# Optimization experiments

Measured on AMD Instinct MI355X. Metric: run time of the kernel, lower is better.

## Reference

```python
import jax, jax.numpy as jnp
import numpy as np

N, D, H1, H2 = 8192, 768, 512, 256


def _nig_head(x, W1, b1, W2, b2, Wh, bh):
    # Linear -> GELU -> (dropout=id) -> Linear -> GELU -> Linear head, then softplus transforms
    h = jax.nn.gelu(x @ W1 + b1, approximate=False)
    h = jax.nn.gelu(h @ W2 + b2, approximate=False)
    r = h @ Wh + bh  # [N, 4]
    mu = r[:, 0]
    v = jax.nn.softplus(r[:, 1]) + 1e-6
    a = jax.nn.softplus(r[:, 2]) + 1.0 + 1e-6
    b = jax.nn.softplus(r[:, 3]) + 1e-6
    return mu, v, a, b


def setup_inputs() -> dict:
    key = jax.random.key(0)
    ks = jax.random.split(key, 16)
    f32 = jnp.float32
    sd = 1.0 / np.sqrt(D)

    def lin(k, din, dout):
        kw, kb = jax.random.split(k)
        W = jax.random.normal(kw, (din, dout), f32) * (1.0 / np.sqrt(din))
        b = jax.random.normal(kb, (dout,), f32) * 0.01
        return W, b

    X = jax.random.normal(ks[0], (N, D), f32)
    Wq = jax.random.normal(ks[1], (D, D), f32) * sd
    Wk = jax.random.normal(ks[2], (D, D), f32) * sd
    Wg, bg = lin(ks[3], D, D)
    gam = jnp.array(1.0, f32)
    ih_W1, ih_b1 = lin(ks[4], D, H1)
    ih_W2, ih_b2 = lin(ks[5], H1, H2)
    ih_Wh, ih_bh = lin(ks[6], H2, 4)
    fh_W1, fh_b1 = lin(ks[7], D, H1)
    fh_W2, fh_b2 = lin(ks[8], H1, H2)
    fh_Wh, fh_bh = lin(ks[9], H2, 4)
    return {
        "X": X, "Wq": Wq, "Wk": Wk, "Wg": Wg, "bg": bg, "gam": gam,
        "ih_W1": ih_W1, "ih_b1": ih_b1, "ih_W2": ih_W2, "ih_b2": ih_b2,
        "ih_Wh": ih_Wh, "ih_bh": ih_bh,
        "fh_W1": fh_W1, "fh_b1": fh_b1, "fh_W2": fh_W2, "fh_b2": fh_b2,
        "fh_Wh": fh_Wh, "fh_bh": fh_bh,
    }


def reference(X, Wq, Wk, Wg, bg, gam,
              ih_W1, ih_b1, ih_W2, ih_b2, ih_Wh, ih_bh,
              fh_W1, fh_b1, fh_W2, fh_b2, fh_Wh, fh_bh):
    # initial NIG head -> epistemic uncertainty -> gate
    m0, v0, a0, b0 = _nig_head(X, ih_W1, ih_b1, ih_W2, ih_b2, ih_Wh, ih_bh)
    u0 = b0 / jnp.maximum(a0 - 1.0, 1e-8)
    G = 1.0 - gam * jax.nn.sigmoid(u0)  # [N]

    # dense attention adjacency
    scale = jnp.sqrt(jnp.asarray(D, X.dtype))
    Q = X @ Wq
    K = X @ Wk
    A = jax.nn.softmax(Q @ K.T / scale, axis=-1)  # [N, N]

    # uncertainty outer-product gate + row renormalization
    A_gated = A * G[None, :] * G[:, None]
    Dinv = 1.0 / jnp.maximum(A_gated.sum(-1, keepdims=True), 1e-8)

    # degree-normalized GCN aggregation + linear + GELU
    M = jax.nn.gelu((A_gated * Dinv) @ X @ Wg + bg, approximate=False)

    # final NIG head on residual
    mu, v, al, be = _nig_head(X + M, fh_W1, fh_b1, fh_W2, fh_b2, fh_Wh, fh_bh)
    return (m0, v0, a0, b0, mu, v, al, be)
```

## Files before the change

### kernel.cpp

```cpp
#include <hip/hip_runtime.h>
#include <hip/hip_bf16.h>
#include <hip/hip_fp8.h>
#include <math.h>
#include <stdint.h>
#include <stddef.h>


#define NT    8192
#define DD    768
#define DH1   512
#define DH2   256
#define PANEL 4096
#define NPAN  (NT / PANEL)

typedef __attribute__((ext_vector_type(8))) short  short8;
typedef __attribute__((ext_vector_type(4))) float  f32x4;
typedef __attribute__((ext_vector_type(2))) long   longx2;

#define MFMA16(a, b, c) __builtin_amdgcn_mfma_f32_16x16x32_bf16((a), (b), (c), 0, 0, 0)
#define MFMAF8(a, b, c) __builtin_amdgcn_mfma_f32_16x16x32_fp8_fp8((a), (b), (c), 0, 0, 0)

__device__ __forceinline__ float bf2f(__hip_bfloat16 x) { return __bfloat162float(x); }
__device__ __forceinline__ __hip_bfloat16 f2bf(float x) { return __float2bfloat16(x); }
__device__ __forceinline__ uint8_t f2fp8(float x) { return __hip_fp8_e4m3(x).__x; }

__device__ __forceinline__ float gelu_f(float x) {
    return 0.5f * x * (1.0f + erff(x * 0.7071067811865476f));
}
__device__ __forceinline__ float softplus_f(float x) {
    return (x > 20.0f) ? x : log1pf(expf(x));
}

__device__ __forceinline__ void gload16(const void* g, void* l) {
    __builtin_amdgcn_global_load_lds(
        (const __attribute__((address_space(1))) void*)g,
        (__attribute__((address_space(3))) void*)l, 16, 0, 0);
}

template <int N>
__device__ __forceinline__ void wait_barrier() {
    asm volatile("s_waitcnt vmcnt(%0)\n\ts_barrier" :: "i"(N) : "memory");
}
__device__ __forceinline__ void plain_barrier() {
    asm volatile("s_barrier" ::: "memory");
}

__device__ __forceinline__ void xcd_remap(int& bx, int& by) {
    const int nbx = gridDim.x, nby = gridDim.y;
    if ((nby & 7) == 0) {
        const int lin = by * nbx + bx;
        const int x   = lin & 7;
        const int s   = lin >> 3;
        bx = s % nbx;
        by = x + 8 * (s / nbx);
    }
}

template <int EPI, bool SPLIT, int TM, int TN>
__global__ __launch_bounds__(256)
void gemm_bt(const __hip_bfloat16* __restrict__ Ahi, const __hip_bfloat16* __restrict__ Alo, int lda,
             const __hip_bfloat16* __restrict__ Bhi, const __hip_bfloat16* __restrict__ Blo, int ldb,
             __hip_bfloat16* __restrict__ obf_hi, __hip_bfloat16* __restrict__ obf_lo,
             uint8_t* __restrict__ of8, int ldc,
             const float* __restrict__ bias, int K)
{
    constexpr int NB  = SPLIT ? 2 : 1;
    constexpr int WRM = (TM == 128 && TN == 128) ? 2 : (TM == 128 ? 4 : 2);
    constexpr int WCN = 4 / WRM;
    constexpr int WTM = TM / WRM;
    constexpr int WTN = TN / WCN;
    constexpr int MI  = WTM / 16;
    constexpr int NI  = WTN / 16;
    constexpr int PA  = TM / 64;
    constexpr int PB  = TN / 64;
    constexpr int LPI = (PA + PB) * NB;

    __shared__ __align__(16) __hip_bfloat16 As[NB][3][TM * 32];
    __shared__ __align__(16) __hip_bfloat16 Bs[NB][3][TN * 32];

    const int tid  = threadIdx.x;
    const int wave = tid >> 6;
    const int lane = tid & 63;
    int bx = blockIdx.x, by = blockIdx.y;
    xcd_remap(bx, by);
    const int tm = by * TM;
    const int tn = bx * TN;

    const int srow  = tid >> 2;
    const int sgcol = ((tid & 3) ^ ((srow >> 1) & 3)) * 8;
    const int lofs  = srow * 32 + (tid & 3) * 8;

    size_t aoffs[PA], boffs[PB];
#pragma unroll
    for (int p = 0; p < PA; ++p) aoffs[p] = (size_t)(tm + p * 64 + srow) * lda + sgcol;
#pragma unroll
    for (int p = 0; p < PB; ++p) boffs[p] = (size_t)(tn + p * 64 + srow) * ldb + sgcol;

    auto stage = [&](int k0, int buf) {
#pragma unroll
        for (int p = 0; p < PA; ++p)
            gload16(Ahi + aoffs[p] + k0, &As[0][buf][p * 2048 + lofs]);
#pragma unroll
        for (int p = 0; p < PB; ++p)
            gload16(Bhi + boffs[p] + k0, &Bs[0][buf][p * 2048 + lofs]);
        if constexpr (SPLIT) {
#pragma unroll
            for (int p = 0; p < PA; ++p)
                gload16(Alo + aoffs[p] + k0, &As[1][buf][p * 2048 + lofs]);
#pragma unroll
            for (int p = 0; p < PB; ++p)
                gload16(Blo + boffs[p] + k0, &Bs[1][buf][p * 2048 + lofs]);
        }
    };

    f32x4 acc[MI][NI];
#pragma unroll
    for (int i = 0; i < MI; ++i)
#pragma unroll
        for (int j = 0; j < NI; ++j) {
            f32x4 z = {0.0f, 0.0f, 0.0f, 0.0f};
            acc[i][j] = z;
        }

    const int wm   = (wave / WCN) * WTM;
    const int wn   = (wave % WCN) * WTN;
    const int l16  = lane & 15;
    const int quad = lane >> 4;
    const int rchunk = (quad ^ ((l16 >> 1) & 3)) * 8;
    const int arow0  = (wm + l16) * 32 + rchunk;
    const int brow0  = (wn + l16) * 32 + rchunk;

    const int nIter = K >> 5;
    stage(0, 0);
    if (nIter > 1) stage(32, 1);
    for (int k = 0; k < nIter; ++k) {
        const int cb = k % 3;
        if (k + 2 < nIter) {
            stage((k + 2) << 5, (k + 2) % 3);
            wait_barrier<2 * LPI>();
        } else if (k + 1 < nIter) {
            wait_barrier<LPI>();
        } else {
            wait_barrier<0>();
        }

        short8 ah[MI], bh[NI];
#pragma unroll
        for (int i = 0; i < MI; ++i) ah[i] = *(const short8*)&As[0][cb][arow0 + i * 512];
#pragma unroll
        for (int j = 0; j < NI; ++j) bh[j] = *(const short8*)&Bs[0][cb][brow0 + j * 512];
        if constexpr (SPLIT) {
            short8 al[MI], bl[NI];
#pragma unroll
            for (int i = 0; i < MI; ++i) al[i] = *(const short8*)&As[1][cb][arow0 + i * 512];
#pragma unroll
            for (int j = 0; j < NI; ++j) bl[j] = *(const short8*)&Bs[1][cb][brow0 + j * 512];
#pragma unroll
            for (int mi = 0; mi < MI; ++mi)
#pragma unroll
                for (int ni = 0; ni < NI; ++ni) {
                    acc[mi][ni] = MFMA16(ah[mi], bh[ni], acc[mi][ni]);
                    acc[mi][ni] = MFMA16(ah[mi], bl[ni], acc[mi][ni]);
                    acc[mi][ni] = MFMA16(al[mi], bh[ni], acc[mi][ni]);
                }
        } else {
#pragma unroll
            for (int mi = 0; mi < MI; ++mi)
#pragma unroll
                for (int ni = 0; ni < NI; ++ni)
                    acc[mi][ni] = MFMA16(ah[mi], bh[ni], acc[mi][ni]);
        }
        plain_barrier();
    }

    const int rbase = tm + wm + quad * 4;
    const int cbase = tn + wn + l16;

    if constexpr (EPI == 0) {
#pragma unroll
        for (int mi = 0; mi < MI; ++mi)
#pragma unroll
            for (int ni = 0; ni < NI; ++ni) {
                f32x4 v = acc[mi][ni];
                const int col = cbase + ni * 16;
#pragma unroll
                for (int r = 0; r < 4; ++r) {
                    size_t idx = (size_t)(rbase + mi * 16 + r) * ldc + col;
                    if (obf_hi) obf_hi[idx] = f2bf(v[r]);
                    if (of8)    of8[idx]    = f2fp8(v[r]);
                }
            }
    } else {
#pragma unroll
        for (int mi = 0; mi < MI; ++mi)
#pragma unroll
            for (int ni = 0; ni < NI; ++ni) {
                f32x4 v = acc[mi][ni];
                const int col = cbase + ni * 16;
                const float b = bias[col];
#pragma unroll
                for (int r = 0; r < 4; ++r) {
                    float g = gelu_f(v[r] + b);
                    __hip_bfloat16 h = f2bf(g);
                    size_t idx = (size_t)(rbase + mi * 16 + r) * ldc + col;
                    obf_hi[idx] = h;
                    if (obf_lo) obf_lo[idx] = f2bf(g - bf2f(h));
                }
            }
    }
}

template <int EPI, int TM, int TN>
__global__ __launch_bounds__(256)
void gemm_f8(const uint8_t* __restrict__ A, int lda,
             const uint8_t* __restrict__ B, int ldb,
             uint8_t* __restrict__ of8, float* __restrict__ ofp, int ldc,
             const float* __restrict__ Gv, float* __restrict__ Esum,
             float* __restrict__ Tsum, int K, int accin)
{
    constexpr int WRM = (TN == 128) ? 2 : 4;
    constexpr int WCN = 4 / WRM;
    constexpr int WTM = TM / WRM;
    constexpr int WTN = TN / WCN;
    constexpr int MI  = WTM / 16;
    constexpr int NI  = WTN / 16;
    constexpr int PA  = TM / 64;
    constexpr int PB  = TN / 64;
    constexpr int LPI = PA + PB;

    __shared__ __align__(16) uint8_t As[3][TM * 64];
    __shared__ __align__(16) uint8_t Bs[3][TN * 64];

    const int tid  = threadIdx.x;
    const int wave = tid >> 6;
    const int lane = tid & 63;
    int bx = blockIdx.x, by = blockIdx.y;
    xcd_remap(bx, by);
    const int tm = by * TM;
    const int tn = bx * TN;

    const int srow  = tid >> 2;
    const int sgcol = ((tid & 3) ^ ((srow >> 1) & 3)) * 16;
    const int lofs  = tid * 16;

    size_t aoffs[PA], boffs[PB];
#pragma unroll
    for (int p = 0; p < PA; ++p) aoffs[p] = (size_t)(tm + p * 64 + srow) * lda + sgcol;
#pragma unroll
    for (int p = 0; p < PB; ++p) boffs[p] = (size_t)(tn + p * 64 + srow) * ldb + sgcol;

    auto stage = [&](int k0, int buf) {
#pragma unroll
        for (int p = 0; p < PA; ++p)
            gload16(A + aoffs[p] + k0, &As[buf][p * 4096 + lofs]);
#pragma unroll
        for (int p = 0; p < PB; ++p)
            gload16(B + boffs[p] + k0, &Bs[buf][p * 4096 + lofs]);
    };

    f32x4 acc[MI][NI];
#pragma unroll
    for (int i = 0; i < MI; ++i)
#pragma unroll
        for (int j = 0; j < NI; ++j) {
            f32x4 z = {0.0f, 0.0f, 0.0f, 0.0f};
            acc[i][j] = z;
        }

    const int wm   = (wave / WCN) * WTM;
    const int wn   = (wave % WCN) * WTN;
    const int l16  = lane & 15;
    const int quad = lane >> 4;
    const int rchunk = (quad ^ ((l16 >> 1) & 3)) * 16;
    const int arow0  = (wm + l16) * 64 + rchunk;
    const int brow0  = (wn + l16) * 64 + rchunk;

    const int nIter = K >> 6;
    stage(0, 0);
    if (nIter > 1) stage(64, 1);
    for (int k = 0; k < nIter; ++k) {
        const int cb = k % 3;
        if (k + 2 < nIter) {
            stage((k + 2) << 6, (k + 2) % 3);
            wait_barrier<2 * LPI>();
        } else if (k + 1 < nIter) {
            wait_barrier<LPI>();
        } else {
            wait_barrier<0>();
        }

        longx2 a[MI], b[NI];
#pragma unroll
        for (int i = 0; i < MI; ++i) a[i] = *(const longx2*)&As[cb][arow0 + i * 1024];
#pragma unroll
        for (int j = 0; j < NI; ++j) b[j] = *(const longx2*)&Bs[cb][brow0 + j * 1024];
#pragma unroll
        for (int mi = 0; mi < MI; ++mi)
#pragma unroll
            for (int ni = 0; ni < NI; ++ni) {
                acc[mi][ni] = MFMAF8(a[mi][0], b[ni][0], acc[mi][ni]);
                acc[mi][ni] = MFMAF8(a[mi][1], b[ni][1], acc[mi][ni]);
            }
        plain_barrier();
    }

    const int rbase = tm + wm + quad * 4;
    const int cbase = tn + wn + l16;

    if constexpr (EPI == 2) {
        const float SCL = 0.03608439182435161f;
#pragma unroll
        for (int mi = 0; mi < MI; ++mi) {
            float sE[4] = {0.f, 0.f, 0.f, 0.f};
            float sT[4] = {0.f, 0.f, 0.f, 0.f};
#pragma unroll
            for (int ni = 0; ni < NI; ++ni) {
                f32x4 v = acc[mi][ni];
                const int col = cbase + ni * 16;
                const float g = Gv[col];
#pragma unroll
                for (int r = 0; r < 4; ++r) {
                    float we = __expf(v[r] * SCL);
                    float w  = we * g;
                    of8[(size_t)(rbase + mi * 16 + r) * ldc + col] = f2fp8(w);
                    sE[r] += we;
                    sT[r] += w;
                }
            }
#pragma unroll
            for (int st = 1; st < 16; st <<= 1)
#pragma unroll
                for (int r = 0; r < 4; ++r) {
                    sE[r] += __shfl_xor(sE[r], st);
                    sT[r] += __shfl_xor(sT[r], st);
                }
            if (l16 == 0) {
#pragma unroll
                for (int r = 0; r < 4; ++r) {
                    atomicAdd(&Esum[rbase + mi * 16 + r], sE[r]);
                    atomicAdd(&Tsum[rbase + mi * 16 + r], sT[r]);
                }
            }
        }
    } else {
#pragma unroll
        for (int mi = 0; mi < MI; ++mi)
#pragma unroll
            for (int ni = 0; ni < NI; ++ni) {
                f32x4 v = acc[mi][ni];
                const int col = cbase + ni * 16;
#pragma unroll
                for (int r = 0; r < 4; ++r) {
                    size_t idx = (size_t)(rbase + mi * 16 + r) * ldc + col;
                    if (accin) ofp[idx] += v[r];
                    else       ofp[idx]  = v[r];
                }
            }
    }
}

__global__ __launch_bounds__(256)
void transpose_f2b(const float* __restrict__ in, int ldin,
                   __hip_bfloat16* __restrict__ ohi, __hip_bfloat16* __restrict__ olo, int ldout)
{
    __shared__ float t[32][33];
    const int tx = threadIdx.x & 31;
    const int ty = threadIdx.x >> 5;
    const int r0 = blockIdx.y * 32;
    const int c0 = blockIdx.x * 32;
#pragma unroll
    for (int j = 0; j < 32; j += 8)
        t[ty + j][tx] = in[(size_t)(r0 + ty + j) * ldin + c0 + tx];
    __syncthreads();
#pragma unroll
    for (int j = 0; j < 32; j += 8) {
        float x = t[tx][ty + j];
        __hip_bfloat16 h = f2bf(x);
        size_t o = (size_t)(c0 + ty + j) * ldout + r0 + tx;
        ohi[o] = h;
        if (olo) olo[o] = f2bf(x - bf2f(h));
    }
}

__global__ __launch_bounds__(256)
void transpose_f8(const uint8_t* __restrict__ in, int ldin,
                  uint8_t* __restrict__ out, int ldout)
{
    __shared__ uint8_t t[32][33];
    const int tx = threadIdx.x & 31;
    const int ty = threadIdx.x >> 5;
    const int r0 = blockIdx.y * 32;
    const int c0 = blockIdx.x * 32;
#pragma unroll
    for (int j = 0; j < 32; j += 8)
        t[ty + j][tx] = in[(size_t)(r0 + ty + j) * ldin + c0 + tx];
    __syncthreads();
#pragma unroll
    for (int j = 0; j < 32; j += 8)
        out[(size_t)(c0 + ty + j) * ldout + r0 + tx] = t[tx][ty + j];
}

__global__ __launch_bounds__(256)
void cvt_split(const float* __restrict__ in, __hip_bfloat16* __restrict__ hi,
               __hip_bfloat16* __restrict__ lo)
{
    const int i = (blockIdx.x * 256 + threadIdx.x) * 4;
    f32x4 v = *(const f32x4*)(in + i);
#pragma unroll
    for (int k = 0; k < 4; ++k) {
        __hip_bfloat16 h = f2bf(v[k]);
        hi[i + k] = h;
        lo[i + k] = f2bf(v[k] - bf2f(h));
    }
}

__global__ __launch_bounds__(256)
void head_tail(const __hip_bfloat16* __restrict__ H2hi, const __hip_bfloat16* __restrict__ H2lo,
               const float* __restrict__ Wh, const float* __restrict__ bh,
               const float* __restrict__ gamp,
               float* __restrict__ outBase, float* __restrict__ Gout)
{
    __shared__ float sa[64], sb[64];
    const int tid = threadIdx.x;
    const int rl  = tid >> 2;
    const int c   = tid & 3;
    const int row = blockIdx.x * 64 + rl;
    const __hip_bfloat16* hh = H2hi + (size_t)row * DH2;
    const __hip_bfloat16* hl = H2lo ? H2lo + (size_t)row * DH2 : nullptr;
    float acc = bh[c];
    if (hl) {
        for (int k = 0; k < DH2; ++k)
            acc = fmaf(bf2f(hh[k]) + bf2f(hl[k]), Wh[k * 4 + c], acc);
    } else {
        for (int k = 0; k < DH2; ++k)
            acc = fmaf(bf2f(hh[k]), Wh[k * 4 + c], acc);
    }
    float sp = softplus_f(acc);
    if (c == 0) {
        outBase[row] = acc;
    } else if (c == 1) {
        outBase[NT + row] = sp + 1e-6f;
    } else if (c == 2) {
        float a0 = (sp + 1.0f) + 1e-6f;
        outBase[2 * NT + row] = a0;
        if (Gout) sa[rl] = a0 - 1.0f;
    } else {
        float b0 = sp + 1e-6f;
        outBase[3 * NT + row] = b0;
        if (Gout) sb[rl] = b0;
    }
    if (Gout != nullptr) {
        __syncthreads();
        if (c == 0) {
            float u   = sb[rl] / fmaxf(sa[rl], 1e-8f);
            float sig = 1.0f / (1.0f + expf(-u));
            Gout[row] = 1.0f - gamp[0] * sig;
        }
    }
}

__global__ __launch_bounds__(256)
void fuse_y(const float* __restrict__ X, const float* __restrict__ Macc,
            const float* __restrict__ G, const float* __restrict__ E,
            const float* __restrict__ T, const float* __restrict__ bg,
            __hip_bfloat16* __restrict__ Yhi)
{
    const int i   = blockIdx.x * 256 + threadIdx.x;
    const int row = i / DD;
    const int col = i - row * DD;
    const float g = G[row], e = E[row], t = T[row];
    const float denom = fmaxf(g * t / e, 1e-8f);
    const float alpha = g / (e * denom);
    const float m = alpha * Macc[i];
    Yhi[i] = f2bf(X[i] + gelu_f(m + bg[col]));
}

extern "C" void kernel_launch(void* const* d_in, const int* in_sizes, int n_in,
                              void* d_out, int out_size, void* d_ws, size_t ws_size,
                              hipStream_t stream)
{
    (void)in_sizes; (void)n_in; (void)out_size; (void)ws_size;
    const float* X   = (const float*)d_in[0];
    const float* Wq  = (const float*)d_in[1];
    const float* Wk  = (const float*)d_in[2];
    const float* Wg  = (const float*)d_in[3];
    const float* bg  = (const float*)d_in[4];
    const float* gam = (const float*)d_in[5];
    const float* iW1 = (const float*)d_in[6];
    const float* ib1 = (const float*)d_in[7];
    const float* iW2 = (const float*)d_in[8];
    const float* ib2 = (const float*)d_in[9];
    const float* iWh = (const float*)d_in[10];
    const float* ibh = (const float*)d_in[11];
    const float* fW1 = (const float*)d_in[12];
    const float* fb1 = (const float*)d_in[13];
    const float* fW2 = (const float*)d_in[14];
    const float* fb2 = (const float*)d_in[15];
    const float* fWh = (const float*)d_in[16];
    const float* fbh = (const float*)d_in[17];
    float* out = (float*)d_out;

    char* cur = (char*)d_ws;
    auto alloc = [&](size_t bytes) -> char* {
        char* p = cur;
        cur += (bytes + 255) & ~(size_t)255;
        return p;
    };
    typedef __hip_bfloat16 bf;

    char* regA = alloc((size_t)NT * DD * 4 + (size_t)NT * DH1 * 4 + (size_t)NT * DH2 * 4);
    uint8_t* Wp = (uint8_t*)regA;
    bf* Xhi  = (bf*)(regA);
    bf* Xlo  = (bf*)(regA + (size_t)NT * DD * 2);
    bf* H1hi = (bf*)(regA + (size_t)NT * DD * 4);
    bf* H1lo = (bf*)(regA + (size_t)NT * DD * 4 + (size_t)NT * DH1 * 2);
    bf* H2hi = (bf*)(regA + (size_t)NT * DD * 4 + (size_t)NT * DH1 * 4);
    bf* H2lo = (bf*)(regA + (size_t)NT * DD * 4 + (size_t)NT * DH1 * 4 + (size_t)NT * DH2 * 2);

    bf* WqkvT  = (bf*)alloc((size_t)3 * DD * DD * 2);
    bf* iW1hiT = (bf*)alloc((size_t)DH1 * DD * 2);
    bf* iW1loT = (bf*)alloc((size_t)DH1 * DD * 2);
    bf* iW2hiT = (bf*)alloc((size_t)DH2 * DH1 * 2);
    bf* iW2loT = (bf*)alloc((size_t)DH2 * DH1 * 2);
    bf* fW1hiT = (bf*)alloc((size_t)DH1 * DD * 2);
    bf* fW2hiT = (bf*)alloc((size_t)DH2 * DH1 * 2);
    uint8_t* QKVf8 = (uint8_t*)alloc((size_t)NT * 3 * DD);
    uint8_t* VTf8  = (uint8_t*)alloc((size_t)DD * NT);
    float* G    = (float*)alloc((size_t)NT * 4);
    float* E    = (float*)alloc((size_t)NT * 4);
    float* T    = (float*)alloc((size_t)NT * 4);
    float* Macc = (float*)alloc((size_t)NT * DD * 4);
    bf* Yhi    = (bf*)alloc((size_t)NT * DD * 2);

    const dim3 blk(256);

    cvt_split<<<dim3(NT * DD / 1024), blk, 0, stream>>>(X, Xhi, Xlo);
    transpose_f2b<<<dim3(DD / 32, DD / 32), blk, 0, stream>>>(Wq, DD, WqkvT, nullptr, DD);
    transpose_f2b<<<dim3(DD / 32, DD / 32), blk, 0, stream>>>(Wk, DD, WqkvT + (size_t)DD * DD, nullptr, DD);
    transpose_f2b<<<dim3(DD / 32, DD / 32), blk, 0, stream>>>(Wg, DD, WqkvT + (size_t)2 * DD * DD, nullptr, DD);
    transpose_f2b<<<dim3(DH1 / 32, DD / 32), blk, 0, stream>>>(iW1, DH1, iW1hiT, iW1loT, DD);
    transpose_f2b<<<dim3(DH2 / 32, DH1 / 32), blk, 0, stream>>>(iW2, DH2, iW2hiT, iW2loT, DH1);
    transpose_f2b<<<dim3(DH1 / 32, DD / 32), blk, 0, stream>>>(fW1, DH1, fW1hiT, nullptr, DD);
    transpose_f2b<<<dim3(DH2 / 32, DH1 / 32), blk, 0, stream>>>(fW2, DH2, fW2hiT, nullptr, DH1);

    gemm_bt<1, true, 64, 64><<<dim3(DH1 / 64, NT / 64), blk, 0, stream>>>(
        Xhi, Xlo, DD, iW1hiT, iW1loT, DD, H1hi, H1lo, nullptr, DH1, ib1, DD);
    gemm_bt<1, true, 64, 64><<<dim3(DH2 / 64, NT / 64), blk, 0, stream>>>(
        H1hi, H1lo, DH1, iW2hiT, iW2loT, DH1, H2hi, H2lo, nullptr, DH2, ib2, DH1);
    head_tail<<<dim3(NT / 64), blk, 0, stream>>>(H2hi, H2lo, iWh, ibh, gam, out, G);

    gemm_bt<0, false, 128, 128><<<dim3(3 * DD / 128, NT / 128), blk, 0, stream>>>(
        Xhi, nullptr, DD, WqkvT, nullptr, DD, nullptr, nullptr, QKVf8, 3 * DD,
        nullptr, DD);
    transpose_f8<<<dim3(DD / 32, NT / 32), blk, 0, stream>>>(QKVf8 + 2 * DD, 3 * DD, VTf8, NT);

    hipMemsetAsync(E, 0, (size_t)NT * 4, stream);
    hipMemsetAsync(T, 0, (size_t)NT * 4, stream);

    for (int p = 0; p < NPAN; ++p) {
        const uint8_t* Kp = QKVf8 + (size_t)p * PANEL * (3 * DD) + DD;
        gemm_f8<2, 128, 128><<<dim3(PANEL / 128, NT / 128), blk, 0, stream>>>(
            QKVf8, 3 * DD, Kp, 3 * DD, Wp, nullptr, PANEL,
            G + p * PANEL, E, T, DD, 0);
        gemm_f8<3, 128, 64><<<dim3(DD / 64, NT / 128), blk, 0, stream>>>(
            Wp, PANEL, VTf8 + (size_t)p * PANEL, NT, nullptr, Macc, DD,
            nullptr, nullptr, nullptr, PANEL, p > 0 ? 1 : 0);
    }

    fuse_y<<<dim3(NT * DD / 256), blk, 0, stream>>>(X, Macc, G, E, T, bg, Yhi);

    gemm_bt<1, false, 64, 64><<<dim3(DH1 / 64, NT / 64), blk, 0, stream>>>(
        Yhi, nullptr, DD, fW1hiT, nullptr, DD, H1hi, nullptr, nullptr, DH1, fb1, DD);
    gemm_bt<1, false, 64, 64><<<dim3(DH2 / 64, NT / 64), blk, 0, stream>>>(
        H1hi, nullptr, DH1, fW2hiT, nullptr, DH1, H2hi, nullptr, nullptr, DH2, fb2, DH1);
    head_tail<<<dim3(NT / 64), blk, 0, stream>>>(H2hi, nullptr, fWh, fbh, gam, out + 4 * NT, nullptr);
}
```

Baseline: 561.6 us.

## Drop attention panelization, fuse gate-normalize-GELU epilogue, use double buffering

Replaces the two-panel loop with one full-width score GEMM writing an NxN fp8 buffer, followed by one A·V GEMM over K=8192. The gate, row normalisation, GELU and residual are computed in that GEMM's epilogue, so the separate fuse_y kernel and the fp32 Macc accumulator (with its read-modify-write) are gone. Both GEMM kernels also move from triple to double buffering in shared memory, which cuts LDS use but allows less prefetch depth. The cost is a larger 64MB intermediate buffer and a single long-K GEMM with fewer blocks.

Result: faster. 550.6 us (-2.0%).

```diff
diff --git a/kernel.cpp b/kernel.cpp
--- a/kernel.cpp
+++ b/kernel.cpp
@@ -10,8 +10,6 @@
 #define DD    768
 #define DH1   512
 #define DH2   256
-#define PANEL 4096
-#define NPAN  (NT / PANEL)
 
 typedef __attribute__((ext_vector_type(8))) short  short8;
 typedef __attribute__((ext_vector_type(4))) float  f32x4;
@@ -75,8 +73,8 @@
     constexpr int PB  = TN / 64;
     constexpr int LPI = (PA + PB) * NB;
 
-    __shared__ __align__(16) __hip_bfloat16 As[NB][3][TM * 32];
-    __shared__ __align__(16) __hip_bfloat16 Bs[NB][3][TN * 32];
+    __shared__ __align__(16) __hip_bfloat16 As[NB][2][TM * 32];
+    __shared__ __align__(16) __hip_bfloat16 Bs[NB][2][TN * 32];
 
     const int tid  = threadIdx.x;
     const int wave = tid >> 6;
@@ -132,13 +130,10 @@
 
     const int nIter = K >> 5;
     stage(0, 0);
-    if (nIter > 1) stage(32, 1);
     for (int k = 0; k < nIter; ++k) {
-        const int cb = k % 3;
-        if (k + 2 < nIter) {
-            stage((k + 2) << 5, (k + 2) % 3);
-            wait_barrier<2 * LPI>();
-        } else if (k + 1 < nIter) {
+        const int cb = k & 1;
+        if (k + 1 < nIter) {
+            stage((k + 1) << 5, cb ^ 1);
             wait_barrier<LPI>();
         } else {
             wait_barrier<0>();
@@ -214,9 +209,13 @@
 __global__ __launch_bounds__(256)
 void gemm_f8(const uint8_t* __restrict__ A, int lda,
              const uint8_t* __restrict__ B, int ldb,
-             uint8_t* __restrict__ of8, float* __restrict__ ofp, int ldc,
+             uint8_t* __restrict__ of8, int ldc,
              const float* __restrict__ Gv, float* __restrict__ Esum,
-             float* __restrict__ Tsum, int K, int accin)
+             float* __restrict__ Tsum,
+             const float* __restrict__ Xf, const float* __restrict__ bg2,
+             const float* __restrict__ Grow, const float* __restrict__ Erow,
+             const float* __restrict__ Trow,
+             __hip_bfloat16* __restrict__ Yout, int K)
 {
     constexpr int WRM = (TN == 128) ? 2 : 4;
     constexpr int WCN = 4 / WRM;
@@ -228,8 +227,8 @@
     constexpr int PB  = TN / 64;
     constexpr int LPI = PA + PB;
 
-    __shared__ __align__(16) uint8_t As[3][TM * 64];
-    __shared__ __align__(16) uint8_t Bs[3][TN * 64];
+    __shared__ __align__(16) uint8_t As[2][TM * 64];
+    __shared__ __align__(16) uint8_t Bs[2][TN * 64];
 
     const int tid  = threadIdx.x;
     const int wave = tid >> 6;
@@ -277,13 +276,10 @@
 
     const int nIter = K >> 6;
     stage(0, 0);
-    if (nIter > 1) stage(64, 1);
     for (int k = 0; k < nIter; ++k) {
-        const int cb = k % 3;
-        if (k + 2 < nIter) {
-            stage((k + 2) << 6, (k + 2) % 3);
-            wait_barrier<2 * LPI>();
-        } else if (k + 1 < nIter) {
+        const int cb = k & 1;
+        if (k + 1 < nIter) {
+            stage((k + 1) << 6, cb ^ 1);
             wait_barrier<LPI>();
         } else {
             wait_barrier<0>();
@@ -344,18 +340,22 @@
         }
     } else {
 #pragma unroll
-        for (int mi = 0; mi < MI; ++mi)
-#pragma unroll
-            for (int ni = 0; ni < NI; ++ni) {
-                f32x4 v = acc[mi][ni];
-                const int col = cbase + ni * 16;
-#pragma unroll
-                for (int r = 0; r < 4; ++r) {
-                    size_t idx = (size_t)(rbase + mi * 16 + r) * ldc + col;
-                    if (accin) ofp[idx] += v[r];
-                    else       ofp[idx]  = v[r];
+        for (int mi = 0; mi < MI; ++mi) {
+#pragma unroll
+            for (int r = 0; r < 4; ++r) {
+                const int row = rbase + mi * 16 + r;
+                const float g = Grow[row], e = Erow[row], t = Trow[row];
+                const float denom = fmaxf(g * t / e, 1e-8f);
+                const float alpha = g / (e * denom);
+#pragma unroll
+                for (int ni = 0; ni < NI; ++ni) {
+                    const int col = cbase + ni * 16;
+                    const float m = alpha * acc[mi][ni][r];
+                    const size_t idx = (size_t)row * ldc + col;
+                    Yout[idx] = f2bf(Xf[idx] + gelu_f(m + bg2[col]));
                 }
             }
+        }
     }
 }
 
@@ -457,22 +457,6 @@
             Gout[row] = 1.0f - gamp[0] * sig;
         }
     }
-}
-
-__global__ __launch_bounds__(256)
-void fuse_y(const float* __restrict__ X, const float* __restrict__ Macc,
-            const float* __restrict__ G, const float* __restrict__ E,
-            const float* __restrict__ T, const float* __restrict__ bg,
-            __hip_bfloat16* __restrict__ Yhi)
-{
-    const int i   = blockIdx.x * 256 + threadIdx.x;
-    const int row = i / DD;
-    const int col = i - row * DD;
-    const float g = G[row], e = E[row], t = T[row];
-    const float denom = fmaxf(g * t / e, 1e-8f);
-    const float alpha = g / (e * denom);
-    const float m = alpha * Macc[i];
-    Yhi[i] = f2bf(X[i] + gelu_f(m + bg[col]));
 }
 
 extern "C" void kernel_launch(void* const* d_in, const int* in_sizes, int n_in,
@@ -508,7 +492,7 @@
     };
     typedef __hip_bfloat16 bf;
 
-    char* regA = alloc((size_t)NT * DD * 4 + (size_t)NT * DH1 * 4 + (size_t)NT * DH2 * 4);
+    char* regA = alloc((size_t)NT * NT);
     uint8_t* Wp = (uint8_t*)regA;
     bf* Xhi  = (bf*)(regA);
     bf* Xlo  = (bf*)(regA + (size_t)NT * DD * 2);
@@ -529,7 +513,6 @@
     float* G    = (float*)alloc((size_t)NT * 4);
     float* E    = (float*)alloc((size_t)NT * 4);
     float* T    = (float*)alloc((size_t)NT * 4);
-    float* Macc = (float*)alloc((size_t)NT * DD * 4);
     bf* Yhi    = (bf*)alloc((size_t)NT * DD * 2);
 
     const dim3 blk(256);
@@ -557,17 +540,13 @@
     hipMemsetAsync(E, 0, (size_t)NT * 4, stream);
     hipMemsetAsync(T, 0, (size_t)NT * 4, stream);
 
-    for (int p = 0; p < NPAN; ++p) {
-        const uint8_t* Kp = QKVf8 + (size_t)p * PANEL * (3 * DD) + DD;
-        gemm_f8<2, 128, 128><<<dim3(PANEL / 128, NT / 128), blk, 0, stream>>>(
-            QKVf8, 3 * DD, Kp, 3 * DD, Wp, nullptr, PANEL,
-            G + p * PANEL, E, T, DD, 0);
-        gemm_f8<3, 128, 64><<<dim3(DD / 64, NT / 128), blk, 0, stream>>>(
-            Wp, PANEL, VTf8 + (size_t)p * PANEL, NT, nullptr, Macc, DD,
-            nullptr, nullptr, nullptr, PANEL, p > 0 ? 1 : 0);
-    }
-
-    fuse_y<<<dim3(NT * DD / 256), blk, 0, stream>>>(X, Macc, G, E, T, bg, Yhi);
+    gemm_f8<2, 128, 128><<<dim3(NT / 128, NT / 128), blk, 0, stream>>>(
+        QKVf8, 3 * DD, QKVf8 + DD, 3 * DD, Wp, NT,
+        G, E, T, nullptr, nullptr, nullptr, nullptr, nullptr, nullptr, DD);
+
+    gemm_f8<4, 128, 64><<<dim3(DD / 64, NT / 128), blk, 0, stream>>>(
+        Wp, NT, VTf8, NT, nullptr, DD,
+        nullptr, nullptr, nullptr, X, bg, G, E, T, Yhi, NT);
 
     gemm_bt<1, false, 64, 64><<<dim3(DH1 / 64, NT / 64), blk, 0, stream>>>(
         Yhi, nullptr, DD, fW1hiT, nullptr, DD, H1hi, nullptr, nullptr, DH1, fb1, DD);
```
